# Performance work log

Hardware: AMD Instinct MI355X
Metric: run time of the kernel (lower is better)

## Reference

```python
import jax, jax.numpy as jnp
import numpy as np

N_NODES = 100000
N_EDGES = 1600000
IN_FEATS = 256
OUT_FEATS = 128


def setup_inputs() -> dict:
    key = jax.random.key(0)
    k1, k2, k3, k4 = jax.random.split(key, 4)
    feat = jax.random.normal(k1, (N_NODES, IN_FEATS), dtype=jnp.float32)
    W = jax.random.normal(k2, (IN_FEATS, OUT_FEATS), dtype=jnp.float32)
    src = jax.random.randint(k3, (N_EDGES,), 0, N_NODES, dtype=jnp.int64)
    dst = jax.random.randint(k4, (N_EDGES,), 0, N_NODES, dtype=jnp.int64)
    return {"feat": feat, "W": W, "src": src, "dst": dst}


def reference(feat, W, src, dst):
    # h_self = feat @ W  -> [N, out_feats]
    h_self = feat @ W
    # update_all(copy_src('h','m'), sum('m','neigh')): gather source features,
    # scatter-sum at destination nodes (SpMM over the edge list).
    msgs = h_self[src]                                        # [E, out_feats]
    h_neigh = jax.ops.segment_sum(msgs, dst, num_segments=N_NODES)
    # in-degree per node
    degs = jax.ops.segment_sum(jnp.ones(dst.shape, jnp.float32), dst,
                               num_segments=N_NODES)          # [N]
    rst = (h_neigh + h_self) / (degs[:, None] + 1.0)
    return jax.nn.relu(rst)
```

## Files before the change

### kernel.cpp

```cpp
#include <hip/hip_runtime.h>
#include <hip/hip_bf16.h>


#define IN_FEATS 256
#define OUT_FEATS 128
#define NUM_NODES 100000
#define NUM_EDGES 1600000

#define NB 782
#define EC 128
#define CHUNK_E 12500
#define BCAP 3072
#define GEMM_BLOCKS 391

typedef __attribute__((ext_vector_type(8))) short short8;
typedef __attribute__((ext_vector_type(8))) unsigned short ushort8;
typedef __attribute__((ext_vector_type(4))) float f32x4;

static __device__ inline unsigned short f2bfu(float x) {
    union { __hip_bfloat16 h; unsigned short u; } c;
    c.h = __float2bfloat16(x);
    return c.u;
}
static __device__ inline ushort2 f2bfu2(float x, float y) {
    union { __hip_bfloat162 h; ushort2 u; } c;
    c.h = __float22bfloat162_rn(make_float2(x, y));
    return c.u;
}
static __device__ inline float bf2f(unsigned short h) {
    return __uint_as_float((unsigned)h << 16);
}

__global__ __launch_bounds__(256) void convert_hist(
    const float* __restrict__ W, unsigned short* __restrict__ Wt,
    const int* __restrict__ dst, int* __restrict__ counts)
{
    int b = blockIdx.x;
    int t = threadIdx.x;
    if (b < 128) {
        int i = b * 256 + t;
        int n = i >> 8;
        int k = i & 255;
        Wt[i] = f2bfu(W[(size_t)k * OUT_FEATS + n]);
        return;
    }
    int c = b - 128;
    __shared__ int hist[NB];
    for (int i = t; i < NB; i += 256) hist[i] = 0;
    __syncthreads();
    const int4* dp = (const int4*)(dst + c * CHUNK_E);
    for (int i = t; i < CHUNK_E / 4; i += 256) {
        int4 d4 = dp[i];
        atomicAdd(&hist[d4.x >> 7], 1);
        atomicAdd(&hist[d4.y >> 7], 1);
        atomicAdd(&hist[d4.z >> 7], 1);
        atomicAdd(&hist[d4.w >> 7], 1);
    }
    __syncthreads();
    for (int i = t; i < NB; i += 256) counts[c * NB + i] = hist[i];
}

__global__ __launch_bounds__(128) void scan_chunks(
    int* __restrict__ counts, int* __restrict__ bucket_total)
{
    __shared__ int sd[128];
    int b = blockIdx.x, t = threadIdx.x;
    int v = counts[t * NB + b];
    sd[t] = v;
    __syncthreads();
    for (int o = 1; o < 128; o <<= 1) {
        int x = (t >= o) ? sd[t - o] : 0;
        __syncthreads();
        sd[t] += x;
        __syncthreads();
    }
    counts[t * NB + b] = sd[t] - v;
    if (t == 127) bucket_total[b] = sd[127];
}

__global__ __launch_bounds__(256) void scan_buckets(
    const int* __restrict__ bucket_total, int* __restrict__ bucket_base)
{
    __shared__ int sd[256];
    int t = threadIdx.x;
    int base = t * 4;
    int v0 = 0, v1 = 0, v2 = 0, v3 = 0;
    if (base + 3 < NB) {
        int4 v = *(const int4*)&bucket_total[base];
        v0 = v.x; v1 = v.y; v2 = v.z; v3 = v.w;
    } else {
        if (base + 0 < NB) v0 = bucket_total[base + 0];
        if (base + 1 < NB) v1 = bucket_total[base + 1];
        if (base + 2 < NB) v2 = bucket_total[base + 2];
        if (base + 3 < NB) v3 = bucket_total[base + 3];
    }
    int s = v0 + v1 + v2 + v3;
    sd[t] = s;
    __syncthreads();
    for (int o = 1; o < 256; o <<= 1) {
        int x = (t >= o) ? sd[t - o] : 0;
        __syncthreads();
        sd[t] += x;
        __syncthreads();
    }
    int e0 = sd[t] - s, e1 = e0 + v0, e2 = e1 + v1, e3 = e2 + v2;
    if (base + 0 < NB) bucket_base[base + 0] = e0;
    if (base + 1 < NB) bucket_base[base + 1] = e1;
    if (base + 2 < NB) bucket_base[base + 2] = e2;
    if (base + 3 < NB) bucket_base[base + 3] = e3;
}

__global__ __launch_bounds__(512, 4) void gemm_scatter(
    const float* __restrict__ feat, const unsigned short* __restrict__ Wt,
    unsigned short* __restrict__ hself16, int M,
    const int* __restrict__ src, const int* __restrict__ dst,
    const int* __restrict__ counts, const int* __restrict__ bucket_base,
    int* __restrict__ bedges)
{
    __shared__ char smem_raw[65536];
    const int tid = threadIdx.x;

    if (blockIdx.x >= GEMM_BLOCKS) {
        int c = blockIdx.x - GEMM_BLOCKS;
        int* cur = (int*)smem_raw;
        for (int i = tid; i < NB; i += 512)
            cur[i] = bucket_base[i] + counts[c * NB + i];
        __syncthreads();
        const int4* dp = (const int4*)(dst + c * CHUNK_E);
        const int4* sp = (const int4*)(src + c * CHUNK_E);
        for (int i = tid; i < CHUNK_E / 4; i += 512) {
            int4 d4 = dp[i];
            int4 s4 = sp[i];
            int dv[4] = { d4.x, d4.y, d4.z, d4.w };
            int sv[4] = { s4.x, s4.y, s4.z, s4.w };
#pragma unroll
            for (int j = 0; j < 4; ++j) {
                int d = dv[j];
                int slot = atomicAdd(&cur[d >> 7], 1);
                bedges[slot] = sv[j] | ((d & 127) << 17);
            }
        }
        return;
    }

    unsigned short* Bl = (unsigned short*)smem_raw;

    {
        int n = tid >> 2;
        int gbase = (tid & 3) * 8;
#pragma unroll
        for (int j = 0; j < 8; ++j) {
            int g = gbase + j;
            ushort8 v = *(const ushort8*)(Wt + (size_t)n * IN_FEATS + g * 8);
            *(ushort8*)(Bl + n * IN_FEATS + ((g ^ (n & 7)) * 8)) = v;
        }
    }
    __syncthreads();

    const int w  = tid >> 6;
    const int l  = tid & 63;
    const int lf = l & 15;
    const int lg = (l >> 4) & 3;
    const int bm0 = blockIdx.x * 256;
    const int rbase = bm0 + w * 32;

    f32x4 acc[2][8];
#pragma unroll
    for (int mt = 0; mt < 2; ++mt)
#pragma unroll
        for (int nt = 0; nt < 8; ++nt)
            acc[mt][nt] = (f32x4){0.f, 0.f, 0.f, 0.f};

#pragma unroll 2
    for (int k0 = 0; k0 < IN_FEATS; k0 += 32) {
        int k8 = k0 >> 3;
        short8 af[2];
#pragma unroll
        for (int mt = 0; mt < 2; ++mt) {
            int grow = rbase + mt * 16 + lf;
            if (grow < M) {
                const float4* ap = (const float4*)(feat + (size_t)grow * IN_FEATS + k0 + lg * 8);
                float4 f0 = ap[0];
                float4 f1 = ap[1];
                ushort2 c0 = f2bfu2(f0.x, f0.y);
                ushort2 c1 = f2bfu2(f0.z, f0.w);
                ushort2 c2 = f2bfu2(f1.x, f1.y);
                ushort2 c3 = f2bfu2(f1.z, f1.w);
                af[mt] = (short8){ (short)c0.x, (short)c0.y, (short)c1.x, (short)c1.y,
                                   (short)c2.x, (short)c2.y, (short)c3.x, (short)c3.y };
            } else {
                af[mt] = (short8){ 0, 0, 0, 0, 0, 0, 0, 0 };
            }
        }
#pragma unroll
        for (int nh = 0; nh < 2; ++nh) {
            short8 bf[4];
#pragma unroll
            for (int q = 0; q < 4; ++q) {
                int nt = nh * 4 + q;
                int n = nt * 16 + lf;
                int g = (k8 + lg) ^ (lf & 7);
                bf[q] = *(const short8*)(Bl + n * IN_FEATS + g * 8);
            }
#pragma unroll
            for (int q = 0; q < 4; ++q) {
                int nt = nh * 4 + q;
                acc[0][nt] = __builtin_amdgcn_mfma_f32_16x16x32_bf16(af[0], bf[q], acc[0][nt], 0, 0, 0);
                acc[1][nt] = __builtin_amdgcn_mfma_f32_16x16x32_bf16(af[1], bf[q], acc[1][nt], 0, 0, 0);
            }
        }
    }

    __syncthreads();
    unsigned short* ep = (unsigned short*)smem_raw;
#pragma unroll
    for (int mt = 0; mt < 2; ++mt)
#pragma unroll
        for (int nt = 0; nt < 8; ++nt)
#pragma unroll
            for (int r = 0; r < 4; ++r) {
                int row = w * 32 + mt * 16 + lg * 4 + r;
                ep[row * 128 + nt * 16 + lf] = f2bfu(acc[mt][nt][r]);
            }
    __syncthreads();
#pragma unroll
    for (int i = 0; i < 8; ++i) {
        int lrow = w * 32 + i * 4 + (l >> 4);
        ushort8 v = *(const ushort8*)(ep + lrow * 128 + (l & 15) * 8);
        int grow = bm0 + lrow;
        if (grow < M)
            *(ushort8*)(hself16 + (size_t)grow * OUT_FEATS + (l & 15) * 8) = v;
    }
}

__global__ __launch_bounds__(512, 8) void sort_gather(
    const int* __restrict__ bucket_base, const int* __restrict__ bucket_total,
    const int* __restrict__ bedges, const unsigned short* __restrict__ hself16,
    float* __restrict__ out)
{
    __shared__ int sorted[BCAP];
    __shared__ int cnt[128], off[128], cursor[128], sd[128];

    int b = blockIdx.x, t = threadIdx.x;
    int base = bucket_base[b];
    int tot = bucket_total[b];
    if (tot > BCAP) tot = BCAP;
    int nnodes = NUM_NODES - b * 128;
    if (nnodes > 128) nnodes = 128;

    if (t < 128) cnt[t] = 0;
    __syncthreads();
    for (int i = t; i < tot; i += 512)
        atomicAdd(&cnt[bedges[base + i] >> 17], 1);
    __syncthreads();
    if (t < 128) sd[t] = cnt[t];
    __syncthreads();
    for (int o = 1; o < 128; o <<= 1) {
        int x = 0;
        if (t < 128 && t >= o) x = sd[t - o];
        __syncthreads();
        if (t < 128) sd[t] += x;
        __syncthreads();
    }
    if (t < 128) { int e = sd[t] - cnt[t]; off[t] = e; cursor[t] = e; }
    __syncthreads();
    for (int i = t; i < tot; i += 512) {
        int e = bedges[base + i];
        int r = atomicAdd(&cursor[e >> 17], 1);
        sorted[r] = e & 0x1FFFF;
    }
    __syncthreads();

    int w = t >> 6, l = t & 63, lg = l >> 4, lf = l & 15;
    for (int ln = w; ln < nnodes; ln += 8) {
        int beg = off[ln];
        int end = beg + cnt[ln];
        float acc[8];
#pragma unroll
        for (int i = 0; i < 8; ++i) acc[i] = 0.f;
        for (int j0 = beg; j0 < end; j0 += 16) {
            int  jj[4];
            bool pp[4];
            int  ss[4];
#pragma unroll
            for (int q = 0; q < 4; ++q) {
                jj[q] = j0 + q * 4 + lg;
                pp[q] = jj[q] < end;
                ss[q] = pp[q] ? sorted[jj[q]] : 0;
            }
            ushort8 h[4];
#pragma unroll
            for (int q = 0; q < 4; ++q)
                h[q] = *(const ushort8*)(hself16 + (size_t)ss[q] * OUT_FEATS + lf * 8);
#pragma unroll
            for (int q = 0; q < 4; ++q)
                if (pp[q]) {
#pragma unroll
                    for (int i = 0; i < 8; ++i) acc[i] += bf2f(h[q][i]);
                }
        }
#pragma unroll
        for (int i = 0; i < 8; ++i) {
            acc[i] += __shfl_xor(acc[i], 16, 64);
            acc[i] += __shfl_xor(acc[i], 32, 64);
        }
        if (lg == 0) {
            int n = b * 128 + ln;
            float inv = 1.0f / (float)(end - beg + 1);
            ushort8 hs = *(const ushort8*)(hself16 + (size_t)n * OUT_FEATS + lf * 8);
            float v[8];
#pragma unroll
            for (int i = 0; i < 8; ++i)
                v[i] = fmaxf((acc[i] + bf2f(hs[i])) * inv, 0.f);
            float4* op = (float4*)(out + (size_t)n * OUT_FEATS + lf * 8);
            op[0] = make_float4(v[0], v[1], v[2], v[3]);
            op[1] = make_float4(v[4], v[5], v[6], v[7]);
        }
    }
}

extern "C" void kernel_launch(void* const* d_in, const int* in_sizes, int n_in,
                              void* d_out, int out_size, void* d_ws, size_t ws_size,
                              hipStream_t stream) {
    const float* feat = (const float*)d_in[0];
    const float* W    = (const float*)d_in[1];
    const int*   src  = (const int*)d_in[2];
    const int*   dst  = (const int*)d_in[3];
    float* out = (float*)d_out;

    char* ws = (char*)d_ws;
    unsigned short* hself16 = (unsigned short*)ws;
    unsigned short* Wt      = (unsigned short*)(ws + 25600000);
    int* counts       = (int*)(ws + 25665536);
    int* bucket_total = (int*)(ws + 26065920);
    int* bucket_base  = (int*)(ws + 26069120);
    int* bedges       = (int*)(ws + 26072320);

    convert_hist<<<256, 256, 0, stream>>>(W, Wt, dst, counts);
    scan_chunks<<<NB, 128, 0, stream>>>(counts, bucket_total);
    scan_buckets<<<1, 256, 0, stream>>>(bucket_total, bucket_base);
    gemm_scatter<<<GEMM_BLOCKS + EC, 512, 0, stream>>>(
        feat, Wt, hself16, NUM_NODES, src, dst, counts, bucket_base, bedges);
    sort_gather<<<NB, 512, 0, stream>>>(bucket_base, bucket_total, bedges, hself16, out);
}
```

Baseline: 281.9 us.

## Double-buffer feature tiles into LDS via async global_load_lds; read W from global

The A operand (fp32 feature rows) is now staged into LDS with async global-to-LDS loads, double-buffered over k chunks so the next chunk's load overlaps the current chunk's MFMAs. The LDS copy of the bf16 weight matrix is dropped, and B fragments are read directly from global memory, relying on the cache because W is small and shared. This trades LDS B reads for global and cache loads in the inner loop, and adds a barrier every k iteration.

```diff
diff --git a/kernel.cpp b/kernel.cpp
--- a/kernel.cpp
+++ b/kernel.cpp
@@ -110,6 +110,25 @@
     if (base + 3 < NB) bucket_base[base + 3] = e3;
 }
 
+static __device__ inline void stage_chunk(
+    const float* __restrict__ feat, char* smem, int buf,
+    int bm0, int k0, int t, int M)
+{
+#pragma unroll
+    for (int j = 0; j < 4; ++j) {
+        int G = j * 512 + t;
+        int r = G >> 3;
+        int g = G & 7;
+        int srow = bm0 + r;
+        if (srow > M - 1) srow = M - 1;
+        const float* src = feat + (size_t)srow * IN_FEATS + k0 + ((g ^ (r & 7)) << 2);
+        __builtin_amdgcn_global_load_lds(
+            (const __attribute__((address_space(1))) unsigned int*)src,
+            (__attribute__((address_space(3))) unsigned int*)(smem + buf * 32768 + G * 16),
+            16, 0, 0);
+    }
+}
+
 __global__ __launch_bounds__(512, 4) void gemm_scatter(
     const float* __restrict__ feat, const unsigned short* __restrict__ Wt,
     unsigned short* __restrict__ hself16, int M,
@@ -143,26 +162,11 @@
         return;
     }
 
-    unsigned short* Bl = (unsigned short*)smem_raw;
-
-    {
-        int n = tid >> 2;
-        int gbase = (tid & 3) * 8;
-#pragma unroll
-        for (int j = 0; j < 8; ++j) {
-            int g = gbase + j;
-            ushort8 v = *(const ushort8*)(Wt + (size_t)n * IN_FEATS + g * 8);
-            *(ushort8*)(Bl + n * IN_FEATS + ((g ^ (n & 7)) * 8)) = v;
-        }
-    }
-    __syncthreads();
-
     const int w  = tid >> 6;
     const int l  = tid & 63;
     const int lf = l & 15;
     const int lg = (l >> 4) & 3;
     const int bm0 = blockIdx.x * 256;
-    const int rbase = bm0 + w * 32;
 
     f32x4 acc[2][8];
 #pragma unroll
@@ -171,27 +175,33 @@
         for (int nt = 0; nt < 8; ++nt)
             acc[mt][nt] = (f32x4){0.f, 0.f, 0.f, 0.f};
 
-#pragma unroll 2
-    for (int k0 = 0; k0 < IN_FEATS; k0 += 32) {
-        int k8 = k0 >> 3;
+    stage_chunk(feat, smem_raw, 0, bm0, 0, tid, M);
+    __syncthreads();
+
+#pragma unroll
+    for (int kc = 0; kc < 8; ++kc) {
+        const int buf = kc & 1;
+        if (kc < 7)
+            stage_chunk(feat, smem_raw, buf ^ 1, bm0, (kc + 1) * 32, tid, M);
+
+        const int k8 = kc * 4;
+
         short8 af[2];
 #pragma unroll
         for (int mt = 0; mt < 2; ++mt) {
-            int grow = rbase + mt * 16 + lf;
-            if (grow < M) {
-                const float4* ap = (const float4*)(feat + (size_t)grow * IN_FEATS + k0 + lg * 8);
-                float4 f0 = ap[0];
-                float4 f1 = ap[1];
-                ushort2 c0 = f2bfu2(f0.x, f0.y);
-                ushort2 c1 = f2bfu2(f0.z, f0.w);
-                ushort2 c2 = f2bfu2(f1.x, f1.y);
-                ushort2 c3 = f2bfu2(f1.z, f1.w);
-                af[mt] = (short8){ (short)c0.x, (short)c0.y, (short)c1.x, (short)c1.y,
-                                   (short)c2.x, (short)c2.y, (short)c3.x, (short)c3.y };
-            } else {
-                af[mt] = (short8){ 0, 0, 0, 0, 0, 0, 0, 0 };
-            }
-        }
+            int r  = w * 32 + mt * 16 + lf;
+            int rs = r & 7;
+            const char* base = smem_raw + buf * 32768 + r * 128;
+            float4 f0 = *(const float4*)(base + ((((lg << 1) + 0) ^ rs) << 4));
+            float4 f1 = *(const float4*)(base + ((((lg << 1) + 1) ^ rs) << 4));
+            ushort2 c0 = f2bfu2(f0.x, f0.y);
+            ushort2 c1 = f2bfu2(f0.z, f0.w);
+            ushort2 c2 = f2bfu2(f1.x, f1.y);
+            ushort2 c3 = f2bfu2(f1.z, f1.w);
+            af[mt] = (short8){ (short)c0.x, (short)c0.y, (short)c1.x, (short)c1.y,
+                               (short)c2.x, (short)c2.y, (short)c3.x, (short)c3.y };
+        }
+
 #pragma unroll
         for (int nh = 0; nh < 2; ++nh) {
             short8 bf[4];
@@ -199,8 +209,7 @@
             for (int q = 0; q < 4; ++q) {
                 int nt = nh * 4 + q;
                 int n = nt * 16 + lf;
-                int g = (k8 + lg) ^ (lf & 7);
-                bf[q] = *(const short8*)(Bl + n * IN_FEATS + g * 8);
+                bf[q] = *(const short8*)(Wt + (size_t)n * IN_FEATS + (k8 + lg) * 8);
             }
 #pragma unroll
             for (int q = 0; q < 4; ++q) {
@@ -209,9 +218,10 @@
                 acc[1][nt] = __builtin_amdgcn_mfma_f32_16x16x32_bf16(af[1], bf[q], acc[1][nt], 0, 0, 0);
             }
         }
-    }
-
-    __syncthreads();
+
+        __syncthreads();
+    }
+
     unsigned short* ep = (unsigned short*)smem_raw;
 #pragma unroll
     for (int mt = 0; mt < 2; ++mt)
```

Result: no change. 287.1 us (+1.8%).
